# Optimization experiments

Hardware: AMD Instinct MI355X
Metric: run time of the kernel (lower is better)

The kernel has to match this reference:

```python
import jax, jax.numpy as jnp
import numpy as np

B, T, IN, H, SH, OUT, NL = 256, 32, 16, 128, 128, 64, 3


def _glorot_like(key, fan_in, shape):
    # matches torch nn.Linear default init U(-1/sqrt(fan_in), 1/sqrt(fan_in))
    lim = 1.0 / np.sqrt(fan_in)
    return jax.random.uniform(key, shape, jnp.float32, -lim, lim)


def setup_inputs() -> dict:
    key = jax.random.key(0)
    ks = jax.random.split(key, 11)
    return {
        "times": jnp.arange(T, dtype=jnp.int32),                    # grid times 0..T-1 -> min_diff = 1
        "coeffs": jax.random.normal(ks[0], (B, T - 1, 4 * IN), jnp.float32),
        "W_init": _glorot_like(ks[1], IN, (H, IN)),
        "b_init": _glorot_like(ks[1], IN, (H,)),
        "W0": _glorot_like(ks[2], H, (SH, H)),
        "b0": _glorot_like(ks[3], H, (SH,)),
        "Wl": _glorot_like(ks[4], SH, (NL, SH, SH)),
        "bl": _glorot_like(ks[5], SH, (NL, SH)),
        "Wf": _glorot_like(ks[6], SH, (IN * H, SH)),
        "bf": _glorot_like(ks[7], SH, (IN * H,)),
        "W_last": _glorot_like(ks[8], H, (OUT, H)),
        "b_last": _glorot_like(ks[9], H, (OUT,)),
    }


def _cde_func(z, W0, b0, Wl, bl, Wf, bf):
    h = jax.nn.relu(z @ W0.T + b0)
    for i in range(NL):
        h = jax.nn.relu(h @ Wl[i].T + bl[i])
    h = jnp.tanh(h @ Wf.T + bf)
    return h.reshape(z.shape[0], H, IN)


def reference(times, coeffs, W_init, b_init, W0, b0, Wl, bl, Wf, bf, W_last, b_last):
    # torchcde.CubicSpline: chunk coeffs into a, b, two_c, three_d along channels
    a, cb, two_c, three_d = jnp.split(coeffs, 4, axis=-1)  # each (B, T-1, IN)
    x0 = a[:, 0, :]                    # spline.evaluate(interval[0])
    z0 = x0 @ W_init.T + b_init        # fc_init

    def step(z, interval):
        bi, ci, di = interval          # (B, IN) each; dX/dt(frac) = b + two_c*frac + three_d*frac^2
        def g(frac, zz):
            f = _cde_func(zz, W0, b0, Wl, bl, Wf, bf)       # (B, H, IN)
            dx = bi + (ci + di * frac) * frac               # (B, IN)
            return jnp.einsum('bhi,bi->bh', f, dx)
        # torchdiffeq rk4 uses the 3/8-rule (rk4_alt_step_func), dt = min_diff = 1
        third = 1.0 / 3.0
        k1 = g(0.0, z)
        k2 = g(third, z + k1 * third)
        k3 = g(2.0 * third, z + (k2 - k1 * third))
        k4 = g(1.0, z + (k1 - k2 + k3))
        zn = z + (k1 + 3.0 * (k2 + k3) + k4) * 0.125
        return zn, zn

    intervals = (jnp.moveaxis(cb, 1, 0), jnp.moveaxis(two_c, 1, 0), jnp.moveaxis(three_d, 1, 0))
    _, zs = jax.lax.scan(step, z0, intervals)               # (T-1, B, H)
    zt = jnp.moveaxis(jnp.concatenate([z0[None], zs], 0), 0, 1)  # (B, T, H)
    return jax.nn.sigmoid(zt @ W_last.T + b_last)           # (B, T, OUT)
```

## Files before the change

### kernel.cpp

```cpp
#include <hip/hip_runtime.h>

typedef _Float16 half8 __attribute__((ext_vector_type(8)));
typedef _Float16 half4 __attribute__((ext_vector_type(4)));
typedef float f32x4 __attribute__((ext_vector_type(4)));

constexpr int OFF_W0HI   = 0;
constexpr int OFF_W0LO   = 16384;
constexpr int OFF_WL     = 32768;
constexpr int OFF_WFHI   = 131072;
constexpr int OFF_WFLO   = 393216;
constexpr int OFF_WLASTHI = 655360;
constexpr int OFF_WLASTLO = 663552;

constexpr int L_ZS   = 0;
constexpr int L_KS   = 8448;
constexpr int L_DX   = 33792;
constexpr int L_AHI  = 35968;
constexpr int L_BHI  = 40320;
constexpr int L_BIAS = 44672;
constexpr int L_WFP  = 55168;
constexpr int LDS_BYTES = 153472;

__device__ __forceinline__ void cvt_elem(const float* __restrict__ W,
                                         _Float16* __restrict__ hi,
                                         _Float16* __restrict__ lo, int e) {
  int j  = e & 7;
  int l  = (e >> 3) & 63;
  int r  = e >> 9;
  int kc = r & 3;
  int nt = r >> 2;
  int row = nt * 16 + (l & 15);
  int col = kc * 32 + ((l >> 4) << 3) + j;
  float v = W[row * 128 + col];
  _Float16 h = (_Float16)v;
  hi[e] = h;
  lo[e] = (_Float16)(v - (float)h);
}

__global__ __launch_bounds__(256) void prep_kernel(const float* __restrict__ W0,
                                                   const float* __restrict__ Wl,
                                                   const float* __restrict__ Wf,
                                                   const float* __restrict__ Wlast,
                                                   _Float16* __restrict__ ws) {
  int e = blockIdx.x * 256 + threadIdx.x;
  if (e < 16384) {
    cvt_elem(W0, ws + OFF_W0HI, ws + OFF_W0LO, e);
  } else if (e < 65536) {
    int ee = e - 16384;
    int m = ee >> 14;
    ee &= 16383;
    cvt_elem(Wl + m * 16384, ws + OFF_WL + m * 32768,
             ws + OFF_WL + m * 32768 + 16384, ee);
  } else if (e < 327680) {
    cvt_elem(Wf, ws + OFF_WFHI, ws + OFF_WFLO, e - 65536);
  } else if (e < 335872) {
    cvt_elem(Wlast, ws + OFF_WLASTHI, ws + OFF_WLASTLO, e - 327680);
  }
}

__device__ __forceinline__ float swz_xor16(float v) {
  return __int_as_float(__builtin_amdgcn_ds_swizzle(__float_as_int(v), 0x401F));
}

__device__ __forceinline__ void out_gemm(int tt, int gb0, int w, int row, int g,
                                         const float* __restrict__ zS,
                                         const _Float16* __restrict__ ws,
                                         const float* __restrict__ biasS,
                                         float* __restrict__ out) {
  f32x4 acc = *(const f32x4*)(biasS + 2560 + w * 16 + g * 4);
  const int lane = g * 16 + row;
#pragma unroll
  for (int kc = 0; kc < 4; ++kc) {
    const float* zp = zS + row * 132 + kc * 32 + g * 8;
    f32x4 z0 = *(const f32x4*)zp;
    f32x4 z1 = *(const f32x4*)(zp + 4);
    half8 ah, al;
#pragma unroll
    for (int j = 0; j < 4; ++j) {
      _Float16 h = (_Float16)z0[j];
      ah[j] = h; al[j] = (_Float16)(z0[j] - (float)h);
      _Float16 h2 = (_Float16)z1[j];
      ah[4 + j] = h2; al[4 + j] = (_Float16)(z1[j] - (float)h2);
    }
    half8 bh = *(const half8*)(ws + OFF_WLASTHI + w * 2048 + (kc * 64 + lane) * 8);
    half8 bl = *(const half8*)(ws + OFF_WLASTLO + w * 2048 + (kc * 64 + lane) * 8);
    acc = __builtin_amdgcn_mfma_f32_16x16x32_f16(bh, ah, acc, 0, 0, 0);
    acc = __builtin_amdgcn_mfma_f32_16x16x32_f16(bh, al, acc, 0, 0, 0);
    acc = __builtin_amdgcn_mfma_f32_16x16x32_f16(bl, ah, acc, 0, 0, 0);
  }
  f32x4 res;
#pragma unroll
  for (int r = 0; r < 4; ++r) {
    float e0 = __builtin_amdgcn_exp2f(-1.4426950408889634f * acc[r]);
    res[r] = __builtin_amdgcn_rcpf(1.f + e0);
  }
  *(f32x4*)(out + ((size_t)(gb0 + row) * 32 + tt) * 64 + w * 16 + g * 4) = res;
}

__global__ __launch_bounds__(512) void cde_kernel(
    const float* __restrict__ coeffs, const float* __restrict__ W_init,
    const float* __restrict__ b_init, const float* __restrict__ b0,
    const float* __restrict__ bl, const float* __restrict__ bf,
    const float* __restrict__ b_last, const _Float16* __restrict__ ws,
    float* __restrict__ out) {
  extern __shared__ char smem[];
  float* zS    = (float*)(smem + L_ZS);
  float* kS    = (float*)(smem + L_KS);
  float* dxS   = (float*)(smem + L_DX);
  _Float16* bufAHi = (_Float16*)(smem + L_AHI);
  _Float16* bufBHi = (_Float16*)(smem + L_BHI);
  float* biasS = (float*)(smem + L_BIAS);
  _Float16* wfP = (_Float16*)(smem + L_WFP);

  const int tid = threadIdx.x;
  const int w = tid >> 6;
  const int lane = tid & 63;
  const int row = lane & 15;
  const int g = lane >> 4;
  const int gb0 = blockIdx.x * 16;

  for (int e = tid; e < 2624; e += 512) {
    float v;
    if (e < 128)       v = b0[e];
    else if (e < 512)  v = bl[e - 128];
    else if (e < 2560) v = bf[e - 512];
    else               v = b_last[e - 2560];
    biasS[e] = v;
  }
  for (int e = tid; e < 2048; e += 512) {
    int b = e >> 7, n = e & 127;
    const float* cr = coeffs + (size_t)(gb0 + b) * (31 * 64);
    float s0 = b_init[n];
#pragma unroll
    for (int i = 0; i < 16; ++i) s0 += cr[i] * W_init[n * 16 + i];
    zS[b * 132 + n] = s0;
  }
  if (tid >= 256) {
    int e = tid - 256;
    int b = e >> 4, i = e & 15;
    const float* cr = coeffs + (size_t)(gb0 + b) * 31 * 64;
    dxS[i * 17 + b] = cr[16 + i];
  }
#pragma unroll
  for (int itS = 0; itS < 3; ++itS)
#pragma unroll
    for (int kc = 0; kc < 4; ++kc) {
      half8 v = *(const half8*)(ws + OFF_WFHI + (w * 16 + 4 + itS) * 2048 +
                                (kc * 64 + lane) * 8);
      *(half8*)(wfP + (((w * 3 + itS) * 4 + kc) * 64 + lane) * 8) = v;
    }

  half8 w0h[4], w1h[4], w2h[4], w3h[4], pwf[16];
  {
#pragma unroll
    for (int kc = 0; kc < 4; ++kc) {
      w0h[kc] = *(const half8*)(ws + OFF_W0HI + w * 2048 + (kc * 64 + lane) * 8);
      w1h[kc] = *(const half8*)(ws + OFF_WL + w * 2048 + (kc * 64 + lane) * 8);
      w2h[kc] = *(const half8*)(ws + OFF_WL + 32768 + w * 2048 + (kc * 64 + lane) * 8);
      w3h[kc] = *(const half8*)(ws + OFF_WL + 65536 + w * 2048 + (kc * 64 + lane) * 8);
    }
#pragma unroll
    for (int it = 0; it < 4; ++it)
#pragma unroll
      for (int kc = 0; kc < 4; ++kc)
        pwf[it * 4 + kc] = *(const half8*)(ws + OFF_WFHI + (w * 16 + it) * 2048 +
                                           (kc * 64 + lane) * 8);
#pragma unroll
    for (int kc = 0; kc < 4; ++kc) {
      asm volatile("" : "+v"(w0h[kc]), "+v"(w1h[kc]), "+v"(w2h[kc]), "+v"(w3h[kc]));
      asm volatile("" : "+v"(pwf[kc]), "+v"(pwf[4 + kc]), "+v"(pwf[8 + kc]),
                        "+v"(pwf[12 + kc]));
    }
  }

  auto hiddenHi = [&](const half8* bh, const _Float16* srcHi, _Float16* dstHi,
                      const float* bias) {
    int n0 = w * 16 + g * 4;
    f32x4 a0 = *(const f32x4*)(bias + n0);
    f32x4 a1 = {0.f, 0.f, 0.f, 0.f};
    half8 f0 = *(const half8*)(srcHi + row * 136 + 0 * 32 + g * 8);
    half8 f1 = *(const half8*)(srcHi + row * 136 + 1 * 32 + g * 8);
    half8 f2 = *(const half8*)(srcHi + row * 136 + 2 * 32 + g * 8);
    half8 f3 = *(const half8*)(srcHi + row * 136 + 3 * 32 + g * 8);
    a0 = __builtin_amdgcn_mfma_f32_16x16x32_f16(bh[0], f0, a0, 0, 0, 0);
    a1 = __builtin_amdgcn_mfma_f32_16x16x32_f16(bh[2], f2, a1, 0, 0, 0);
    a0 = __builtin_amdgcn_mfma_f32_16x16x32_f16(bh[1], f1, a0, 0, 0, 0);
    a1 = __builtin_amdgcn_mfma_f32_16x16x32_f16(bh[3], f3, a1, 0, 0, 0);
    f32x4 acc = a0 + a1;
    half4 hq;
#pragma unroll
    for (int r = 0; r < 4; ++r)
      hq[r] = (_Float16)fmaxf(acc[r], 0.f);
    *(half4*)(dstHi + row * 136 + n0) = hq;
  };

  __syncthreads();

  if (w < 4) out_gemm(0, gb0, w, row, g, zS, ws, biasS, out);

#pragma unroll 1
  for (int t = 0; t < 31; ++t) {
#pragma unroll 1
    for (int s = 0; s < 4; ++s) {
      {
        int b = tid >> 5;
        int c = (tid & 31) * 4;
        float* zp = zS + b * 132 + c;
        f32x4 z = *(const f32x4*)zp;
        f32x4 v = z;
        if (s == 1) {
          f32x4 k1 = *(const f32x4*)(kS + b * 132 + c);
          v = z + k1 * (1.f / 3.f);
        } else if (s == 2) {
          f32x4 k1 = *(const f32x4*)(kS + b * 132 + c);
          f32x4 k2 = *(const f32x4*)(kS + (16 + b) * 132 + c);
          v = z + k2 - k1 * (1.f / 3.f);
        } else if (s == 3) {
          f32x4 k1 = *(const f32x4*)(kS + b * 132 + c);
          f32x4 k2 = *(const f32x4*)(kS + (16 + b) * 132 + c);
          f32x4 k3 = *(const f32x4*)(kS + (32 + b) * 132 + c);
          v = z + k1 - k2 + k3;
          *(f32x4*)zp = z + 0.125f * (k1 + 3.f * (k2 + k3));
        }
        half4 hi;
#pragma unroll
        for (int j = 0; j < 4; ++j) hi[j] = (_Float16)v[j];
        *(half4*)(bufAHi + b * 136 + c) = hi;
      }
      __syncthreads();

      hiddenHi(w0h, bufAHi, bufBHi, biasS);
      __syncthreads();
      hiddenHi(w1h, bufBHi, bufAHi, biasS + 128);
      __syncthreads();
      hiddenHi(w2h, bufAHi, bufBHi, biasS + 256);
      __syncthreads();
      hiddenHi(w3h, bufBHi, bufAHi, biasS + 384);
      __syncthreads();

      if (tid >= 256) {
        int sn = (s + 1) & 3;
        int tn = t + (s == 3);
        if (tn < 31) {
          int e = tid - 256;
          int b = e >> 4, i = e & 15;
          const float* cr = coeffs + ((size_t)(gb0 + b) * 31 + tn) * 64;
          float frac = (sn == 3) ? 1.f : sn * (1.f / 3.f);
          dxS[(((s & 1) ^ 1) * 272) + i * 17 + b] =
              cr[16 + i] + (cr[32 + i] + cr[48 + i] * frac) * frac;
        }
      }

      float dxr[4], dx2[4];
#pragma unroll
      for (int r = 0; r < 4; ++r) {
        dxr[r] = dxS[(s & 1) * 272 + (g * 4 + r) * 17 + row];
        dx2[r] = dxr[r] + dxr[r];
      }
      half8 Ah[4];
#pragma unroll
      for (int kc = 0; kc < 4; ++kc)
        Ah[kc] = *(const half8*)(bufAHi + row * 136 + kc * 32 + g * 8);

      auto g5tile = [&](int it, const half8* bh4) {
        int nt = w * 16 + it;
        f32x4 acc = *(const f32x4*)(biasS + 512 + nt * 16 + g * 4);
#pragma unroll
        for (int kc = 0; kc < 4; ++kc)
          acc = __builtin_amdgcn_mfma_f32_16x16x32_f16(bh4[kc], Ah[kc], acc, 0, 0, 0);
        float tr[4];
#pragma unroll
        for (int r = 0; r < 4; ++r) {
          float e2 = __builtin_amdgcn_exp2f(2.8853900817779268f * acc[r]);
          float rc = __builtin_amdgcn_rcpf(e2 + 1.f);
          tr[r] = __builtin_fmaf(-dx2[r], rc, dxr[r]);
        }
        float sA = (tr[0] + tr[1]) + (tr[2] + tr[3]);
        float sB = sA + swz_xor16(sA);
        float sC = sB + __shfl_xor(sB, 32);
        if (lane < 16) {
          if (s < 3) kS[(s * 16 + lane) * 132 + nt] = sC;
          else       zS[lane * 132 + nt] += 0.125f * sC;
        }
      };

#pragma unroll
      for (int it = 0; it < 4; ++it) g5tile(it, pwf + it * 4);
#pragma unroll
      for (int itS = 0; itS < 3; ++itS) {
        half8 bh4[4];
#pragma unroll
        for (int kc = 0; kc < 4; ++kc)
          bh4[kc] = *(const half8*)(wfP + (((w * 3 + itS) * 4 + kc) * 64 + lane) * 8);
        g5tile(4 + itS, bh4);
      }
      {
        const _Float16* bp = ws + OFF_WFHI + (w * 16 + 7) * 2048;
#pragma unroll 3
        for (int it = 7; it < 16; ++it) {
          half8 bh4[4];
#pragma unroll
          for (int kc = 0; kc < 4; ++kc)
            bh4[kc] = *(const half8*)(bp + (kc * 64 + lane) * 8);
          g5tile(it, bh4);
          bp += 2048;
        }
      }
      __syncthreads();
    }
    if (w < 4) out_gemm(t + 1, gb0, w, row, g, zS, ws, biasS, out);
  }
}

extern "C" void kernel_launch(void* const* d_in, const int* in_sizes, int n_in,
                              void* d_out, int out_size, void* d_ws, size_t ws_size,
                              hipStream_t stream) {
  const float* coeffs = (const float*)d_in[1];
  const float* W_init = (const float*)d_in[2];
  const float* b_init = (const float*)d_in[3];
  const float* W0     = (const float*)d_in[4];
  const float* b0     = (const float*)d_in[5];
  const float* Wl     = (const float*)d_in[6];
  const float* bl     = (const float*)d_in[7];
  const float* Wf     = (const float*)d_in[8];
  const float* bf     = (const float*)d_in[9];
  const float* Wlast  = (const float*)d_in[10];
  const float* b_last = (const float*)d_in[11];
  _Float16* ws = (_Float16*)d_ws;
  float* out = (float*)d_out;

  (void)hipFuncSetAttribute((const void*)cde_kernel,
                            hipFuncAttributeMaxDynamicSharedMemorySize,
                            LDS_BYTES);
  prep_kernel<<<1312, 256, 0, stream>>>(W0, Wl, Wf, Wlast, ws);
  cde_kernel<<<16, 512, LDS_BYTES, stream>>>(coeffs, W_init, b_init, b0, bl, bf,
                                             b_last, ws, out);
}
```

Baseline: 881.4 us.

## Fuse RK stage-input computation into final GEMM epilogue, removing one barrier per stage

Each stage's next RK input (z plus a combination of the k's) is now computed in the epilogue of the last GEMM tile, which writes it straight into a ping-pong fp16 buffer. This removes the separate elementwise pass and one __syncthreads per RK stage, and drops the k3 storage from LDS. The state update is moved into stage 2, and k3 is folded into the input computation, which changes where partial sums live and adds more per-lane epilogue work.

```diff
diff --git a/kernel.cpp b/kernel.cpp
--- a/kernel.cpp
+++ b/kernel.cpp
@@ -14,12 +14,13 @@
 
 constexpr int L_ZS   = 0;
 constexpr int L_KS   = 8448;
-constexpr int L_DX   = 33792;
-constexpr int L_AHI  = 35968;
-constexpr int L_BHI  = 40320;
-constexpr int L_BIAS = 44672;
-constexpr int L_WFP  = 55168;
-constexpr int LDS_BYTES = 153472;
+constexpr int L_DX   = 25344;
+constexpr int L_A0   = 27520;
+constexpr int L_A1   = 31872;
+constexpr int L_B    = 36224;
+constexpr int L_BIAS = 40576;
+constexpr int L_WFP  = 51072;
+constexpr int LDS_BYTES = 149376;
 
 __device__ __forceinline__ void cvt_elem(const float* __restrict__ W,
                                          _Float16* __restrict__ hi,
@@ -107,8 +108,9 @@
   float* zS    = (float*)(smem + L_ZS);
   float* kS    = (float*)(smem + L_KS);
   float* dxS   = (float*)(smem + L_DX);
-  _Float16* bufAHi = (_Float16*)(smem + L_AHI);
-  _Float16* bufBHi = (_Float16*)(smem + L_BHI);
+  _Float16* bufA0 = (_Float16*)(smem + L_A0);
+  _Float16* bufA1 = (_Float16*)(smem + L_A1);
+  _Float16* bufB  = (_Float16*)(smem + L_B);
   float* biasS = (float*)(smem + L_BIAS);
   _Float16* wfP = (_Float16*)(smem + L_WFP);
 
@@ -134,6 +136,7 @@
 #pragma unroll
     for (int i = 0; i < 16; ++i) s0 += cr[i] * W_init[n * 16 + i];
     zS[b * 132 + n] = s0;
+    bufA0[b * 136 + n] = (_Float16)s0;
   }
   if (tid >= 256) {
     int e = tid - 256;
@@ -202,40 +205,16 @@
   for (int t = 0; t < 31; ++t) {
 #pragma unroll 1
     for (int s = 0; s < 4; ++s) {
-      {
-        int b = tid >> 5;
-        int c = (tid & 31) * 4;
-        float* zp = zS + b * 132 + c;
-        f32x4 z = *(const f32x4*)zp;
-        f32x4 v = z;
-        if (s == 1) {
-          f32x4 k1 = *(const f32x4*)(kS + b * 132 + c);
-          v = z + k1 * (1.f / 3.f);
-        } else if (s == 2) {
-          f32x4 k1 = *(const f32x4*)(kS + b * 132 + c);
-          f32x4 k2 = *(const f32x4*)(kS + (16 + b) * 132 + c);
-          v = z + k2 - k1 * (1.f / 3.f);
-        } else if (s == 3) {
-          f32x4 k1 = *(const f32x4*)(kS + b * 132 + c);
-          f32x4 k2 = *(const f32x4*)(kS + (16 + b) * 132 + c);
-          f32x4 k3 = *(const f32x4*)(kS + (32 + b) * 132 + c);
-          v = z + k1 - k2 + k3;
-          *(f32x4*)zp = z + 0.125f * (k1 + 3.f * (k2 + k3));
-        }
-        half4 hi;
-#pragma unroll
-        for (int j = 0; j < 4; ++j) hi[j] = (_Float16)v[j];
-        *(half4*)(bufAHi + b * 136 + c) = hi;
-      }
-      __syncthreads();
-
-      hiddenHi(w0h, bufAHi, bufBHi, biasS);
-      __syncthreads();
-      hiddenHi(w1h, bufBHi, bufAHi, biasS + 128);
-      __syncthreads();
-      hiddenHi(w2h, bufAHi, bufBHi, biasS + 256);
-      __syncthreads();
-      hiddenHi(w3h, bufBHi, bufAHi, biasS + 384);
+      _Float16* bufP = (s & 1) ? bufA1 : bufA0;
+      _Float16* bufN = (s & 1) ? bufA0 : bufA1;
+
+      hiddenHi(w0h, bufP, bufB, biasS);
+      __syncthreads();
+      hiddenHi(w1h, bufB, bufP, biasS + 128);
+      __syncthreads();
+      hiddenHi(w2h, bufP, bufB, biasS + 256);
+      __syncthreads();
+      hiddenHi(w3h, bufB, bufP, biasS + 384);
       __syncthreads();
 
       if (tid >= 256) {
@@ -260,7 +239,7 @@
       half8 Ah[4];
 #pragma unroll
       for (int kc = 0; kc < 4; ++kc)
-        Ah[kc] = *(const half8*)(bufAHi + row * 136 + kc * 32 + g * 8);
+        Ah[kc] = *(const half8*)(bufP + row * 136 + kc * 32 + g * 8);
 
       auto g5tile = [&](int it, const half8* bh4) {
         int nt = w * 16 + it;
@@ -279,8 +258,24 @@
         float sB = sA + swz_xor16(sA);
         float sC = sB + __shfl_xor(sB, 32);
         if (lane < 16) {
-          if (s < 3) kS[(s * 16 + lane) * 132 + nt] = sC;
-          else       zS[lane * 132 + nt] += 0.125f * sC;
+          float z = zS[lane * 132 + nt];
+          if (s == 0) {
+            kS[lane * 132 + nt] = sC;
+            bufN[lane * 136 + nt] = (_Float16)(z + sC * (1.f / 3.f));
+          } else if (s == 1) {
+            float k1 = kS[lane * 132 + nt];
+            kS[(16 + lane) * 132 + nt] = sC;
+            bufN[lane * 136 + nt] = (_Float16)(z + sC - k1 * (1.f / 3.f));
+          } else if (s == 2) {
+            float k1 = kS[lane * 132 + nt];
+            float k2 = kS[(16 + lane) * 132 + nt];
+            zS[lane * 132 + nt] = z + 0.125f * (k1 + 3.f * (k2 + sC));
+            bufN[lane * 136 + nt] = (_Float16)(z + k1 - k2 + sC);
+          } else {
+            float zn = z + 0.125f * sC;
+            zS[lane * 132 + nt] = zn;
+            bufN[lane * 136 + nt] = (_Float16)zn;
+          }
         }
       };
 
```

After: 952.7 us. +8.1%, slower.
